# Kernel optimization log

Hardware: AMD Instinct MI355X
Metric: run time of the kernel (lower is better)

## Reference

```python
import jax, jax.numpy as jnp
import numpy as np

N_NODES = 200000
N_EDGES = 6400000
NUM_FEATURES = 128


def _glorot(key, fan_in, fan_out):
    return jax.random.normal(key, (fan_in, fan_out), jnp.float32) * (1.0 / np.sqrt(fan_in))


def gcn_conv(x, src, dst, W, b):
    """PyG GCNConv: h = D^{-1/2}(A+I)D^{-1/2} (x @ W) + b, self-loops added."""
    n = x.shape[0]
    ones = jnp.ones(src.shape, x.dtype)
    # degree after adding self-loops: 1 + in-degree (edges flow src -> dst)
    deg = 1.0 + jax.ops.segment_sum(ones, dst, num_segments=n)
    dinv = jax.lax.rsqrt(deg)  # deg >= 1, safe
    h = x @ W  # [n, out]
    norm = dinv[src] * dinv[dst]  # [E]
    msg = h[src] * norm[:, None]
    agg = jax.ops.segment_sum(msg, dst, num_segments=n)
    agg = agg + h * (dinv * dinv)[:, None]  # self-loop contribution
    return agg + b


def setup_inputs() -> dict:
    key = jax.random.key(0)
    ks = jax.random.split(key, 16)
    x = jax.random.normal(ks[0], (N_NODES, NUM_FEATURES), jnp.float32)
    edge_index = jax.random.randint(ks[1], (2, N_EDGES), 0, N_NODES, dtype=jnp.int64)
    params = {
        'W1': _glorot(ks[2], NUM_FEATURES, 64), 'b1': jnp.zeros((64,), jnp.float32),
        'W2': _glorot(ks[3], 64, 32),           'b2': jnp.zeros((32,), jnp.float32),
        'W3': _glorot(ks[4], 32, 16),           'b3': jnp.zeros((16,), jnp.float32),
        'Wsk02': _glorot(ks[5], NUM_FEATURES, 32), 'bsk02': jnp.zeros((32,), jnp.float32),
        'Wsk13': _glorot(ks[6], 64, 16),           'bsk13': jnp.zeros((16,), jnp.float32),
        'Wlin': _glorot(ks[7], 16, 1),             'blin': jnp.zeros((1,), jnp.float32),
    }
    return {'x': x, 'edge_index': edge_index, **params}


def reference(x, edge_index, W1, b1, W2, b2, W3, b3, Wsk02, bsk02, Wsk13, bsk13, Wlin, blin):
    # Dropout is identity in eval mode.
    src, dst = edge_index[0], edge_index[1]
    h1 = jax.nn.relu(gcn_conv(x, src, dst, W1, b1))
    h2 = jax.nn.relu(gcn_conv(h1, src, dst, W2, b2) + x @ Wsk02 + bsk02)
    h3 = jax.nn.relu(gcn_conv(h2, src, dst, W3, b3) + h1 @ Wsk13 + bsk13)
    return jax.nn.sigmoid(h3 @ Wlin + blin)  # [N, 1]
```

## Files before the change

kernel.cpp:

```cpp
#include <hip/hip_runtime.h>
#include <hip/hip_fp16.h>
#include <math.h>

#define MAXB 1024
#define MAXCB 128
#define TILE1 8192
#define SCAT_T 512
#define EPT1 (TILE1 / SCAT_T)
#define LCAP 13568
#define GCHUNK 4096

typedef _Float16 f16x8 __attribute__((ext_vector_type(8)));
typedef float f32x4 __attribute__((ext_vector_type(4)));


__device__ __forceinline__ unsigned int pack_f16(float a, float b) {
    __half2 h = __floats2half2_rn(a, b);
    return *reinterpret_cast<unsigned int*>(&h);
}
__device__ __forceinline__ float f16_lo(unsigned int u) {
    __half2 h = *reinterpret_cast<__half2*>(&u);
    return __low2float(h);
}
__device__ __forceinline__ float f16_hi(unsigned int u) {
    __half2 h = *reinterpret_cast<__half2*>(&u);
    return __high2float(h);
}
__device__ __forceinline__ void acc8(float* a, uint4 u) {
    a[0] += f16_lo(u.x); a[1] += f16_hi(u.x);
    a[2] += f16_lo(u.y); a[3] += f16_hi(u.y);
    a[4] += f16_lo(u.z); a[5] += f16_hi(u.z);
    a[6] += f16_lo(u.w); a[7] += f16_hi(u.w);
}
__device__ __forceinline__ void unpack8(uint4 u, float* v) {
    v[0] = f16_lo(u.x); v[1] = f16_hi(u.x);
    v[2] = f16_lo(u.y); v[3] = f16_hi(u.y);
    v[4] = f16_lo(u.z); v[5] = f16_hi(u.z);
    v[6] = f16_lo(u.w); v[7] = f16_hi(u.w);
}
__device__ __forceinline__ uint4 h2add4(uint4 a, uint4 b) {
    const __half2* pa = reinterpret_cast<const __half2*>(&a);
    const __half2* pb = reinterpret_cast<const __half2*>(&b);
    uint4 r;
    __half2* pr = reinterpret_cast<__half2*>(&r);
#pragma unroll
    for (int i = 0; i < 4; i++) pr[i] = __hadd2(pa[i], pb[i]);
    return r;
}
__device__ __forceinline__ unsigned int pkadd(unsigned int a, unsigned int b) {
    __half2 r = __hadd2(*reinterpret_cast<__half2*>(&a), *reinterpret_cast<__half2*>(&b));
    return *reinterpret_cast<unsigned int*>(&r);
}


__device__ __forceinline__ bool detect64(const int* __restrict__ ei) {
    int lane = threadIdx.x & 63;
    unsigned long long m = __ballot(ei[2 * lane + 1] != 0);
    return m == 0ull;
}

__device__ __forceinline__ int load_src(const int* ei, int e, bool is64, int i) {
    return is64 ? ei[2 * i] : ei[i];
}
__device__ __forceinline__ int load_dst(const int* ei, int e, bool is64, int i) {
    return is64 ? ei[2 * e + 2 * i] : ei[e + i];
}


__global__ __launch_bounds__(256) void bin_count(const int* __restrict__ ei, int e,
                                                 int shift, int* __restrict__ gcnt) {
    __shared__ int h[MAXB];
    for (int i = threadIdx.x; i < MAXB; i += 256) h[i] = 0;
    bool is64 = detect64(ei);
    __syncthreads();
    int stride = gridDim.x * 256;
    for (int i = blockIdx.x * 256 + threadIdx.x; i < e; i += stride) {
        int d = load_dst(ei, e, is64, i);
        atomicAdd(&h[d >> shift], 1);
    }
    __syncthreads();
    for (int i = threadIdx.x; i < MAXB; i += 256)
        if (h[i]) atomicAdd(&gcnt[i], h[i]);
}


__global__ void bin_scan_init(const int* __restrict__ gcnt, int nb, int ncb,
                              int* __restrict__ base, int* __restrict__ gcursor,
                              int* __restrict__ gcur1) {
    __shared__ int sh[1024];
    __shared__ int ex[1024];
    int t = threadIdx.x;
    int v = (t < nb) ? gcnt[t] : 0;
    sh[t] = v;
    __syncthreads();
    for (int off = 1; off < 1024; off <<= 1) {
        int x = (t >= off) ? sh[t - off] : 0;
        __syncthreads();
        sh[t] += x;
        __syncthreads();
    }
    int excl = sh[t] - v;
    ex[t] = excl;
    if (t < nb) {
        base[t] = excl;
        gcursor[t] = excl;
        if (t == nb - 1) base[nb] = sh[t];
    }
    __syncthreads();
    if (t < ncb) gcur1[t] = ex[8 * t];
}


__global__ __launch_bounds__(SCAT_T) void scatter_coarse(const int* __restrict__ ei, int e,
                                                         int shift,
                                                         int* __restrict__ gcur1,
                                                         unsigned int* __restrict__ gpk1) {
    __shared__ int hist[MAXCB];
    __shared__ int lbase[MAXCB];
    __shared__ int delta[MAXCB];
    __shared__ int cur[MAXCB];
    __shared__ unsigned int sbuf[TILE1];
    __shared__ unsigned char sbkt[TILE1];
    __shared__ int sh[SCAT_T];

    const int t = threadIdx.x;
    const int pkshift = shift + 3;
    const int pkmask = (1 << pkshift) - 1;
    const bool is64 = detect64(ei);
    const int tile0 = blockIdx.x * TILE1;
    const int cnt = min(TILE1, e - tile0);

    for (int i = t; i < MAXCB; i += SCAT_T) hist[i] = 0;
    __syncthreads();

    unsigned int pk[EPT1];
    int bk[EPT1];
#pragma unroll
    for (int k = 0; k < EPT1; k++) {
        int g = tile0 + k * SCAT_T + t;
        bk[k] = -1;
        if (g < e) {
            int s = load_src(ei, e, is64, g);
            int d = load_dst(ei, e, is64, g);
            pk[k] = ((unsigned int)s << pkshift) | (unsigned int)(d & pkmask);
            bk[k] = d >> pkshift;
            atomicAdd(&hist[bk[k]], 1);
        }
    }
    __syncthreads();

    {
        int v = (t < MAXCB) ? hist[t] : 0;
        sh[t] = v;
        __syncthreads();
        for (int off = 1; off < SCAT_T; off <<= 1) {
            int x = (t >= off) ? sh[t - off] : 0;
            __syncthreads();
            sh[t] += x;
            __syncthreads();
        }
        if (t < MAXCB) lbase[t] = sh[t] - v;
    }
    __syncthreads();

    if (t < MAXCB) {
        int c = hist[t];
        if (c > 0) delta[t] = atomicAdd(&gcur1[t], c) - lbase[t];
        cur[t] = lbase[t];
    }
    __syncthreads();

#pragma unroll
    for (int k = 0; k < EPT1; k++) {
        if (bk[k] >= 0) {
            int p = atomicAdd(&cur[bk[k]], 1);
            sbuf[p] = pk[k];
            sbkt[p] = (unsigned char)bk[k];
        }
    }
    __syncthreads();

    for (int i = t; i < cnt; i += SCAT_T)
        gpk1[delta[sbkt[i]] + i] = sbuf[i];
}


__global__ __launch_bounds__(SCAT_T) void scatter_fine(const unsigned int* __restrict__ gpk1,
                                                       const int* __restrict__ base,
                                                       int nbkt, int shift,
                                                       int* __restrict__ gcursor,
                                                       unsigned int* __restrict__ gpk2) {
    __shared__ int hist[8];
    __shared__ int lbase[8];
    __shared__ int delta[8];
    __shared__ int cur[8];
    __shared__ unsigned int sbuf[TILE1];
    __shared__ unsigned char sbkt[TILE1];

    const int t = threadIdx.x;
    const int cb = blockIdx.x >> 3;
    const int s = blockIdx.x & 7;
    const int f0 = 8 * cb;
    const int fhiIdx = min(f0 + 8, nbkt);
    const int lo = base[f0];
    const int hi = base[fhiIdx];
    const int len = hi - lo;
    const int slo = lo + (int)((long long)len * s / 8);
    const int shi = lo + (int)((long long)len * (s + 1) / 8);

    for (int tile0 = slo; tile0 < shi; tile0 += TILE1) {
        const int cnt = min(TILE1, shi - tile0);
        if (t < 8) hist[t] = 0;
        __syncthreads();

        unsigned int pk[EPT1];
        int bk[EPT1];
#pragma unroll
        for (int k = 0; k < EPT1; k++) {
            int li = k * SCAT_T + t;
            bk[k] = -1;
            if (li < cnt) {
                pk[k] = gpk1[tile0 + li];
                bk[k] = (pk[k] >> shift) & 7;
                atomicAdd(&hist[bk[k]], 1);
            }
        }
        __syncthreads();

        if (t == 0) {
            int run = 0;
            for (int f = 0; f < 8; f++) { lbase[f] = run; run += hist[f]; }
        }
        __syncthreads();
        if (t < 8) {
            int c = hist[t];
            if (c > 0) delta[t] = atomicAdd(&gcursor[f0 + t], c) - lbase[t];
            cur[t] = lbase[t];
        }
        __syncthreads();

#pragma unroll
        for (int k = 0; k < EPT1; k++) {
            if (bk[k] >= 0) {
                int p = atomicAdd(&cur[bk[k]], 1);
                sbuf[p] = pk[k];
                sbkt[p] = (unsigned char)bk[k];
            }
        }
        __syncthreads();

        for (int i = t; i < cnt; i += SCAT_T)
            gpk2[delta[sbkt[i]] + i] = sbuf[i];
        __syncthreads();
    }
}


__global__ __launch_bounds__(256) void bucket_build(const unsigned int* __restrict__ gpk,
                                                    const int* __restrict__ base, int shift,
                                                    int n, int e, float* __restrict__ dinv,
                                                    int* __restrict__ row_ptr,
                                                    int* __restrict__ col) {
    __shared__ int lcol[LCAP];
    __shared__ int dc[MAXB];
    __shared__ int cur[MAXB];
    __shared__ int sh[256];
    const int t = threadIdx.x;
    const int b = blockIdx.x;
    const int pkshift = shift + 3;
    const int mask = (1 << shift) - 1;
    const int width = 1 << shift;
    const int node0 = b << shift;
    const int nc = min(width, n - node0);
    const int lo = base[b], hi = base[b + 1];
    const int ecnt = hi - lo;

    for (int i = t; i < width; i += 256) dc[i] = 0;
    __syncthreads();
    for (int j = lo + t; j < hi; j += 256)
        atomicAdd(&dc[gpk[j] & mask], 1);
    __syncthreads();
    {
        int b4 = t * 4;
        int v0 = (b4 + 0 < width) ? dc[b4 + 0] : 0;
        int v1 = (b4 + 1 < width) ? dc[b4 + 1] : 0;
        int v2 = (b4 + 2 < width) ? dc[b4 + 2] : 0;
        int v3 = (b4 + 3 < width) ? dc[b4 + 3] : 0;
        int s = v0 + v1 + v2 + v3;
        sh[t] = s;
        __syncthreads();
        for (int off = 1; off < 256; off <<= 1) {
            int x = (t >= off) ? sh[t - off] : 0;
            __syncthreads();
            sh[t] += x;
            __syncthreads();
        }
        int excl = sh[t] - s;
        int pf[4] = {excl, excl + v0, excl + v0 + v1, excl + v0 + v1 + v2};
        int vv[4] = {v0, v1, v2, v3};
#pragma unroll
        for (int q = 0; q < 4; q++) {
            int i = b4 + q;
            if (i < nc) {
                row_ptr[node0 + i] = lo + pf[q];
                dinv[node0 + i] = rsqrtf(1.0f + (float)vv[q]);
            }
            if (i < width) cur[i] = pf[q];
        }
    }
    if (b == gridDim.x - 1 && t == 0) row_ptr[n] = e;
    __syncthreads();

    if (ecnt <= LCAP) {
        for (int j = lo + t; j < hi; j += 256) {
            unsigned int v = gpk[j];
            int p = atomicAdd(&cur[v & mask], 1);
            lcol[p] = (int)(v >> pkshift);
        }
        __syncthreads();
        for (int j = t; j < ecnt; j += 256)
            col[lo + j] = lcol[j];
    } else {
        for (int j = lo + t; j < hi; j += 256) {
            unsigned int v = gpk[j];
            int p = atomicAdd(&cur[v & mask], 1);
            col[lo + p] = (int)(v >> pkshift);
        }
    }
}


__global__ void prep_w(const float* __restrict__ W1, const float* __restrict__ Wsk02,
                       const float* __restrict__ W2, const float* __restrict__ Wsk13,
                       const float* __restrict__ W3, unsigned short* __restrict__ wt) {
    int i = blockIdx.x * 256 + threadIdx.x;
    float v;
    if (i < 12288) {
        int c = i >> 7, k = i & 127;
        v = (c < 64) ? W1[k * 64 + c] : Wsk02[k * 32 + (c - 64)];
    } else if (i < 15360) {
        int j = i - 12288;
        int c = j >> 6, k = j & 63;
        v = (c < 32) ? W2[k * 32 + c] : Wsk13[k * 16 + (c - 32)];
    } else if (i < 15872) {
        int j = i - 15360;
        int c = j >> 5, k = j & 31;
        v = W3[k * 16 + c];
    } else return;
    wt[i] = (unsigned short)pack_f16(v, 0.f);
}


template <int K, int CO1, int CO2, bool AHALF>
__global__ __launch_bounds__(256) void gemm_mfma(const void* __restrict__ Av,
                                                 const unsigned short* __restrict__ wt,
                                                 const float* __restrict__ dinv,
                                                 unsigned int* __restrict__ out1,
                                                 float* __restrict__ out2, int n) {
    constexpr int N = CO1 + CO2;
    constexpr int NCT = N / 16;
    constexpr int NK = K / 32;
    constexpr int CHK = K / 8;
    constexpr int SWZ = (CHK - 1) < 15 ? (CHK - 1) : 15;
    __shared__ __align__(16) unsigned char Ash[64 * K * 2];
    __shared__ __align__(16) unsigned char Bsh[N * K * 2];

    const int t = threadIdx.x;
    const int row0 = blockIdx.x * 64;

    for (int i = t; i < 64 * CHK; i += 256) {
        int r = i / CHK, c = i % CHK;
        int row = row0 + r;
        uint4 w{0u, 0u, 0u, 0u};
        if (row < n) {
            if (AHALF) {
                w = *reinterpret_cast<const uint4*>(
                    (const unsigned short*)Av + (size_t)row * K + c * 8);
            } else {
                const float* xr = (const float*)Av + (size_t)row * K + c * 8;
                float4 p = *reinterpret_cast<const float4*>(xr);
                float4 q = *reinterpret_cast<const float4*>(xr + 4);
                w.x = pack_f16(p.x, p.y); w.y = pack_f16(p.z, p.w);
                w.z = pack_f16(q.x, q.y); w.w = pack_f16(q.z, q.w);
            }
        }
        int addr = i * 16;
        addr ^= ((r & SWZ) << 4);
        *reinterpret_cast<uint4*>(&Ash[addr]) = w;
    }
    for (int i = t; i < N * CHK; i += 256) {
        int cc = i / CHK;
        uint4 w = *reinterpret_cast<const uint4*>(&wt[(i / CHK) * K + (i % CHK) * 8]);
        int addr = i * 16;
        addr ^= ((cc & SWZ) << 4);
        *reinterpret_cast<uint4*>(&Bsh[addr]) = w;
    }
    __syncthreads();

    const int wv = t >> 6;
    const int lane = t & 63;
    const int lrow = wv * 16 + (lane & 15);
    const int kb = (lane >> 4) * 16;

    f16x8 afr[NK];
#pragma unroll
    for (int s = 0; s < NK; s++) {
        int addr = lrow * (2 * K) + s * 64 + kb;
        addr ^= ((lrow & SWZ) << 4);
        afr[s] = *reinterpret_cast<const f16x8*>(&Ash[addr]);
    }

    f32x4 acc[NCT];
#pragma unroll
    for (int ct = 0; ct < NCT; ct++) acc[ct] = f32x4{0.f, 0.f, 0.f, 0.f};

#pragma unroll
    for (int ct = 0; ct < NCT; ct++) {
        int cc = ct * 16 + (lane & 15);
#pragma unroll
        for (int s = 0; s < NK; s++) {
            int addr = cc * (2 * K) + s * 64 + kb;
            addr ^= ((cc & SWZ) << 4);
            f16x8 bfr = *reinterpret_cast<const f16x8*>(&Bsh[addr]);
            acc[ct] = __builtin_amdgcn_mfma_f32_16x16x32_f16(afr[s], bfr, acc[ct], 0, 0, 0);
        }
    }

    const int rbase = row0 + wv * 16 + (lane >> 4) * 4;
    const int cidx = lane & 15;
    float dn[4];
#pragma unroll
    for (int r = 0; r < 4; r++) dn[r] = (rbase + r < n) ? dinv[rbase + r] : 0.f;

#pragma unroll
    for (int ct = 0; ct < NCT; ct++) {
        int col = ct * 16 + cidx;
        if (col < CO1) {
#pragma unroll
            for (int r = 0; r < 4; r++) {
                float v = acc[ct][r] * dn[r];
                float o = __shfl_xor(v, 1);
                int row = rbase + r;
                if (!(lane & 1) && row < n)
                    out1[(size_t)row * (CO1 / 2) + ct * 8 + cidx / 2] = pack_f16(v, o);
            }
        } else if (CO2 > 0) {
#pragma unroll
            for (int r = 0; r < 4; r++) {
                int row = rbase + r;
                if (row < n) out2[(size_t)row * CO2 + (col - CO1)] = acc[ct][r];
            }
        }
    }
}


template <int F, bool FINAL, bool PACKOUT>
__global__ __launch_bounds__(256) void gather_combine(
    const uint4* __restrict__ hp4, const int* __restrict__ row_ptr,
    const int* __restrict__ col, const float* __restrict__ dinv,
    const float* __restrict__ bias, const float* __restrict__ sk,
    const float* __restrict__ bsk, void* __restrict__ outv,
    const float* __restrict__ Wlin, const float* __restrict__ blin, int n) {
    constexpr int L = F / 8;
    constexpr int EPW = 64 / L;
    int wid = (blockIdx.x * blockDim.x + threadIdx.x) >> 6;
    int lane = threadIdx.x & 63;
    if (wid >= n) return;
    int s = lane / L;
    int el = lane % L;
    int start = row_ptr[wid];
    int end = row_ptr[wid + 1];

    float a[8] = {0.f, 0.f, 0.f, 0.f, 0.f, 0.f, 0.f, 0.f};
    const uint4 z4{0u, 0u, 0u, 0u};
    for (int j = start + s; j < end; j += 4 * EPW) {
        int j1 = j + EPW, j2 = j + 2 * EPW, j3 = j + 3 * EPW;
        bool v1 = j1 < end, v2 = j2 < end, v3 = j3 < end;
        int c0 = col[j];
        int c1 = col[v1 ? j1 : j];
        int c2 = col[v2 ? j2 : j];
        int c3 = col[v3 ? j3 : j];
        uint4 u0 = hp4[(size_t)c0 * L + el];
        uint4 u1 = hp4[(size_t)c1 * L + el];
        uint4 u2 = hp4[(size_t)c2 * L + el];
        uint4 u3 = hp4[(size_t)c3 * L + el];
        if (!v1) u1 = z4;
        if (!v2) u2 = z4;
        if (!v3) u3 = z4;
        uint4 t01 = h2add4(u0, u1);
        uint4 t23 = h2add4(u2, u3);
        acc8(a, h2add4(t01, t23));
    }

#pragma unroll
    for (int m = L; m < 64; m <<= 1) {
#pragma unroll
        for (int q = 0; q < 8; q++) a[q] += __shfl_xor(a[q], m);
    }

    if (lane < L) {
        float dn = dinv[wid];
        uint4 us = hp4[(size_t)wid * L + el];
        float v[8];
        unpack8(us, v);
        float4 b0 = *reinterpret_cast<const float4*>(&bias[8 * el]);
        float4 b1 = *reinterpret_cast<const float4*>(&bias[8 * el + 4]);
        float o[8];
        o[0] = dn * a[0] + v[0] * dn + b0.x;
        o[1] = dn * a[1] + v[1] * dn + b0.y;
        o[2] = dn * a[2] + v[2] * dn + b0.z;
        o[3] = dn * a[3] + v[3] * dn + b0.w;
        o[4] = dn * a[4] + v[4] * dn + b1.x;
        o[5] = dn * a[5] + v[5] * dn + b1.y;
        o[6] = dn * a[6] + v[6] * dn + b1.z;
        o[7] = dn * a[7] + v[7] * dn + b1.w;
        if (sk) {
            float4 s0 = *reinterpret_cast<const float4*>(&sk[(size_t)wid * F + 8 * el]);
            float4 s1 = *reinterpret_cast<const float4*>(&sk[(size_t)wid * F + 8 * el + 4]);
            float4 k0 = *reinterpret_cast<const float4*>(&bsk[8 * el]);
            float4 k1 = *reinterpret_cast<const float4*>(&bsk[8 * el + 4]);
            o[0] += s0.x + k0.x; o[1] += s0.y + k0.y;
            o[2] += s0.z + k0.z; o[3] += s0.w + k0.w;
            o[4] += s1.x + k1.x; o[5] += s1.y + k1.y;
            o[6] += s1.z + k1.z; o[7] += s1.w + k1.w;
        }
#pragma unroll
        for (int q = 0; q < 8; q++) o[q] = fmaxf(o[q], 0.f);
        if (FINAL) {
            float4 wl0 = *reinterpret_cast<const float4*>(&Wlin[8 * el]);
            float4 wl1 = *reinterpret_cast<const float4*>(&Wlin[8 * el + 4]);
            float d = o[0] * wl0.x + o[1] * wl0.y + o[2] * wl0.z + o[3] * wl0.w +
                      o[4] * wl1.x + o[5] * wl1.y + o[6] * wl1.z + o[7] * wl1.w;
            d += __shfl_xor(d, 1);
            if (el == 0) ((float*)outv)[wid] = 1.0f / (1.0f + expf(-(d + blin[0])));
        } else if (PACKOUT) {
            uint4 pk{pack_f16(o[0], o[1]), pack_f16(o[2], o[3]),
                     pack_f16(o[4], o[5]), pack_f16(o[6], o[7])};
            ((uint4*)outv)[(size_t)wid * L + el] = pk;
        } else {
            float* out = (float*)outv;
            float4 w0{o[0], o[1], o[2], o[3]};
            float4 w1{o[4], o[5], o[6], o[7]};
            *reinterpret_cast<float4*>(&out[(size_t)wid * F + 8 * el]) = w0;
            *reinterpret_cast<float4*>(&out[(size_t)wid * F + 8 * el + 4]) = w1;
        }
    }
}


template <int F, bool FINAL, bool PACKOUT>
__global__ __launch_bounds__(256) void gather_tpn(
    const uint4* __restrict__ hp4, const int* __restrict__ row_ptr,
    const int* __restrict__ col, const float* __restrict__ dinv,
    const float* __restrict__ bias, const float* __restrict__ sk,
    const float* __restrict__ bsk, void* __restrict__ outv,
    const float* __restrict__ Wlin, const float* __restrict__ blin, int n) {
    constexpr int L = F / 8;
    __shared__ int lcol[GCHUNK];
    const int t = threadIdx.x;
    const int node0 = blockIdx.x * 256;
    const int node = node0 + t;
    const int hiN = min(node0 + 256, n);
    const int lo = row_ptr[node0];
    const int hi = row_ptr[hiN];

    int start = 0, end = 0;
    if (node < n) { start = row_ptr[node]; end = row_ptr[node + 1]; }

    unsigned int acc[F / 2];
#pragma unroll
    for (int q = 0; q < F / 2; q++) acc[q] = 0u;

    for (int ch = lo; ch < hi; ch += GCHUNK) {
        int cnt = min(GCHUNK, hi - ch);
        __syncthreads();
        for (int i = t; i < cnt; i += 256) lcol[i] = col[ch + i];
        __syncthreads();
        int s0 = max(start, ch);
        int s1 = min(end, ch + cnt);
        for (int j = s0; j < s1; j++) {
            int c = lcol[j - ch];
            const uint4* rp = hp4 + (size_t)c * L;
            uint4 u[L];
#pragma unroll
            for (int w = 0; w < L; w++) u[w] = rp[w];
#pragma unroll
            for (int w = 0; w < L; w++) {
                acc[4 * w + 0] = pkadd(acc[4 * w + 0], u[w].x);
                acc[4 * w + 1] = pkadd(acc[4 * w + 1], u[w].y);
                acc[4 * w + 2] = pkadd(acc[4 * w + 2], u[w].z);
                acc[4 * w + 3] = pkadd(acc[4 * w + 3], u[w].w);
            }
        }
    }

    if (node < n) {
        float dn = dinv[node];
        const uint4* sp = hp4 + (size_t)node * L;
        float o[F];
#pragma unroll
        for (int w = 0; w < L; w++) {
            uint4 u = sp[w];
            float sv[8];
            unpack8(u, sv);
#pragma unroll
            for (int q = 0; q < 8; q++) {
                int f = w * 8 + q;
                float av = (q & 1) ? f16_hi(acc[4 * w + (q >> 1)])
                                   : f16_lo(acc[4 * w + (q >> 1)]);
                o[f] = dn * (av + sv[q]) + bias[f];
            }
        }
        if (sk) {
#pragma unroll
            for (int f = 0; f < F; f++)
                o[f] += sk[(size_t)node * F + f] + bsk[f];
        }
#pragma unroll
        for (int f = 0; f < F; f++) o[f] = fmaxf(o[f], 0.f);

        if (FINAL) {
            float d = blin[0];
#pragma unroll
            for (int f = 0; f < F; f++) d += o[f] * Wlin[f];
            ((float*)outv)[node] = 1.0f / (1.0f + expf(-d));
        } else if (PACKOUT) {
            uint4* o4 = (uint4*)outv + (size_t)node * L;
#pragma unroll
            for (int w = 0; w < L; w++) {
                uint4 pk{pack_f16(o[w * 8 + 0], o[w * 8 + 1]),
                         pack_f16(o[w * 8 + 2], o[w * 8 + 3]),
                         pack_f16(o[w * 8 + 4], o[w * 8 + 5]),
                         pack_f16(o[w * 8 + 6], o[w * 8 + 7])};
                o4[w] = pk;
            }
        }
    }
}


extern "C" void kernel_launch(void* const* d_in, const int* in_sizes, int n_in,
                              void* d_out, int out_size, void* d_ws, size_t ws_size,
                              hipStream_t stream) {
    const float* x     = (const float*)d_in[0];
    const int*   ei    = (const int*)d_in[1];
    const float* W1    = (const float*)d_in[2];
    const float* b1    = (const float*)d_in[3];
    const float* W2    = (const float*)d_in[4];
    const float* b2    = (const float*)d_in[5];
    const float* W3    = (const float*)d_in[6];
    const float* b3    = (const float*)d_in[7];
    const float* Wsk02 = (const float*)d_in[8];
    const float* bsk02 = (const float*)d_in[9];
    const float* Wsk13 = (const float*)d_in[10];
    const float* bsk13 = (const float*)d_in[11];
    const float* Wlin  = (const float*)d_in[12];
    const float* blin  = (const float*)d_in[13];

    const int n = in_sizes[0] / 128;
    const int e = in_sizes[1] / 2;

    int shift = 8;
    while (((n + (1 << shift) - 1) >> shift) > MAXB) shift++;
    const int nbkt = (n + (1 << shift) - 1) >> shift;
    const int ncb = (nbkt + 7) / 8;

    char* p = (char*)d_ws;
    auto alloc = [&](size_t bytes) {
        void* r = (void*)p;
        p += (bytes + 255) / 256 * 256;
        return r;
    };
    int*   gcnt    = (int*)alloc(MAXB * 4);
    int*   base    = (int*)alloc((MAXB + 1) * 4);
    int*   gcursor = (int*)alloc(MAXB * 4);
    int*   gcur1   = (int*)alloc(MAXCB * 4);
    unsigned short* wt = (unsigned short*)alloc(15872 * 2);
    int*   row_ptr = (int*)alloc((size_t)(n + 1) * 4);
    float* dinv    = (float*)alloc((size_t)n * 4);
    int*   col     = (int*)alloc((size_t)e * 4);
    size_t h1b     = (size_t)e * 4 > (size_t)n * 128 ? (size_t)e * 4 : (size_t)n * 128;
    unsigned int* h1 = (unsigned int*)alloc(h1b);
    unsigned int* h2 = (unsigned int*)alloc((size_t)n * 64);
    float* sk02    = (float*)alloc((size_t)n * 32 * 4);
    float* sk13    = (float*)alloc((size_t)n * 16 * 4);
    size_t prebytes = (size_t)e * 4 > (size_t)n * 128 ? (size_t)e * 4 : (size_t)n * 128;
    unsigned int* preb = (unsigned int*)alloc(prebytes);
    unsigned int* gpk1 = h1;
    unsigned int* gpk2 = preb;

    auto cdiv = [](int a, int b) { return (a + b - 1) / b; };

    prep_w<<<62, 256, 0, stream>>>(W1, Wsk02, W2, Wsk13, W3, wt);

    hipMemsetAsync(gcnt, 0, MAXB * 4, stream);
    bin_count<<<1024, 256, 0, stream>>>(ei, e, shift, gcnt);
    bin_scan_init<<<1, 1024, 0, stream>>>(gcnt, nbkt, ncb, base, gcursor, gcur1);
    scatter_coarse<<<cdiv(e, TILE1), SCAT_T, 0, stream>>>(ei, e, shift, gcur1, gpk1);
    scatter_fine<<<ncb * 8, SCAT_T, 0, stream>>>(gpk1, base, nbkt, shift, gcursor, gpk2);
    bucket_build<<<nbkt, 256, 0, stream>>>(gpk2, base, shift, n, e, dinv, row_ptr, col);

    gemm_mfma<128, 64, 32, false><<<cdiv(n, 64), 256, 0, stream>>>(
        x, wt, dinv, preb, sk02, n);
    gather_combine<64, false, true><<<cdiv(n, 4), 256, 0, stream>>>(
        (const uint4*)preb, row_ptr, col, dinv, b1, nullptr, nullptr, h1, nullptr, nullptr, n);

    gemm_mfma<64, 32, 16, true><<<cdiv(n, 64), 256, 0, stream>>>(
        h1, wt + 12288, dinv, preb, sk13, n);
    gather_tpn<32, false, true><<<cdiv(n, 256), 256, 0, stream>>>(
        (const uint4*)preb, row_ptr, col, dinv, b2, sk02, bsk02, h2, nullptr, nullptr, n);

    gemm_mfma<32, 16, 0, true><<<cdiv(n, 64), 256, 0, stream>>>(
        h2, wt + 15360, dinv, preb, sk13, n);
    gather_tpn<16, true, false><<<cdiv(n, 256), 256, 0, stream>>>(
        (const uint4*)preb, row_ptr, col, dinv, b3, sk13, bsk13, d_out, Wlin, blin, n);
}
```

Measured before the change: 532.2 us.

## Split each node's neighbor gather across 4 threads with shuffle reduction and prefetch

The thread-per-node gather kernels now assign T=4 threads to each node. Each thread strides through the node's edge list and prefetches the next neighbor row while accumulating the current one. The partial f16 sums are then combined with xor shuffles, and only lane 0 writes the output. This targets load imbalance and latency from long serial per-thread edge loops, at the cost of 4x more blocks, extra shuffles, and f16 summation in a different order.

After: 456.8 us. 1.17x faster.

```diff
diff --git a/kernel.cpp b/kernel.cpp
--- a/kernel.cpp
+++ b/kernel.cpp
@@ -549,7 +549,7 @@
 }
 
 
-template <int F, bool FINAL, bool PACKOUT>
+template <int F, int T, bool FINAL, bool PACKOUT>
 __global__ __launch_bounds__(256) void gather_tpn(
     const uint4* __restrict__ hp4, const int* __restrict__ row_ptr,
     const int* __restrict__ col, const float* __restrict__ dinv,
@@ -557,11 +557,13 @@
     const float* __restrict__ bsk, void* __restrict__ outv,
     const float* __restrict__ Wlin, const float* __restrict__ blin, int n) {
     constexpr int L = F / 8;
+    constexpr int NPB = 256 / T;
     __shared__ int lcol[GCHUNK];
     const int t = threadIdx.x;
-    const int node0 = blockIdx.x * 256;
-    const int node = node0 + t;
-    const int hiN = min(node0 + 256, n);
+    const int sub = t & (T - 1);
+    const int node0 = blockIdx.x * NPB;
+    const int node = node0 + (t / T);
+    const int hiN = min(node0 + NPB, n);
     const int lo = row_ptr[node0];
     const int hi = row_ptr[hiN];
 
@@ -577,14 +579,32 @@
         __syncthreads();
         for (int i = t; i < cnt; i += 256) lcol[i] = col[ch + i];
         __syncthreads();
-        int s0 = max(start, ch);
-        int s1 = min(end, ch + cnt);
-        for (int j = s0; j < s1; j++) {
-            int c = lcol[j - ch];
-            const uint4* rp = hp4 + (size_t)c * L;
+        int first = start + sub;
+        if (first < ch) first += ((ch - first + T - 1) & ~(T - 1));
+        int last = min(end, ch + cnt);
+        int j = first;
+        if (j < last) {
             uint4 u[L];
-#pragma unroll
-            for (int w = 0; w < L; w++) u[w] = rp[w];
+            {
+                const uint4* rp = hp4 + (size_t)lcol[j - ch] * L;
+#pragma unroll
+                for (int w = 0; w < L; w++) u[w] = rp[w];
+            }
+            for (j += T; j < last; j += T) {
+                uint4 v[L];
+                const uint4* rq = hp4 + (size_t)lcol[j - ch] * L;
+#pragma unroll
+                for (int w = 0; w < L; w++) v[w] = rq[w];
+#pragma unroll
+                for (int w = 0; w < L; w++) {
+                    acc[4 * w + 0] = pkadd(acc[4 * w + 0], u[w].x);
+                    acc[4 * w + 1] = pkadd(acc[4 * w + 1], u[w].y);
+                    acc[4 * w + 2] = pkadd(acc[4 * w + 2], u[w].z);
+                    acc[4 * w + 3] = pkadd(acc[4 * w + 3], u[w].w);
+                }
+#pragma unroll
+                for (int w = 0; w < L; w++) u[w] = v[w];
+            }
 #pragma unroll
             for (int w = 0; w < L; w++) {
                 acc[4 * w + 0] = pkadd(acc[4 * w + 0], u[w].x);
@@ -595,7 +615,16 @@
         }
     }
 
-    if (node < n) {
+#pragma unroll
+    for (int m = 1; m < T; m <<= 1) {
+#pragma unroll
+        for (int q = 0; q < F / 2; q++) {
+            unsigned int o = (unsigned int)__shfl_xor((int)acc[q], m);
+            acc[q] = pkadd(acc[q], o);
+        }
+    }
+
+    if (node < n && sub == 0) {
         float dn = dinv[node];
         const uint4* sp = hp4 + (size_t)node * L;
         float o[F];
@@ -708,11 +737,11 @@
 
     gemm_mfma<64, 32, 16, true><<<cdiv(n, 64), 256, 0, stream>>>(
         h1, wt + 12288, dinv, preb, sk13, n);
-    gather_tpn<32, false, true><<<cdiv(n, 256), 256, 0, stream>>>(
+    gather_tpn<32, 4, false, true><<<cdiv(n, 64), 256, 0, stream>>>(
         (const uint4*)preb, row_ptr, col, dinv, b2, sk02, bsk02, h2, nullptr, nullptr, n);
 
     gemm_mfma<32, 16, 0, true><<<cdiv(n, 64), 256, 0, stream>>>(
         h2, wt + 15360, dinv, preb, sk13, n);
-    gather_tpn<16, true, false><<<cdiv(n, 256), 256, 0, stream>>>(
+    gather_tpn<16, 4, true, false><<<cdiv(n, 64), 256, 0, stream>>>(
         (const uint4*)preb, row_ptr, col, dinv, b3, sk13, bsk13, d_out, Wlin, blin, n);
 }
```
